# Performance work log

Measured on AMD Instinct MI355X. Metric: run time of the kernel, lower is better.

The kernel has to match this reference:

```python
import jax, jax.numpy as jnp
import numpy as np

B, TQ, TKV, NPR, H, D = 4, 1024, 1024, 5, 16, 64
IN, OUT, R, P, NT = 1024, H * D, 64, 4096, 4
KV = NPR + TKV  # prompt tokens prepended to kv sequence


def setup_inputs() -> dict:
    key = jax.random.key(0)
    ks = jax.random.split(key, 20)
    n = lambda k, shp, s: jax.random.normal(k, shp, jnp.float32) * s
    W = 0.02  # weight init scale
    return {
        "pe": n(ks[0], (P, OUT), 1.0),
        "attn_output": n(ks[1], (B, TQ, OUT), 1.0),
        "q": n(ks[2], (B, H, TQ, D), 1.0),
        "kv_query": n(ks[3], (B, TKV, IN), 1.0),
        "attn_mask": jnp.zeros((TQ, KV), jnp.float32),
        "prompt": n(ks[4], (NT, NPR, IN), 1.0),
        "gates": n(ks[5], (1,), 1.0),
        "k_w1": n(ks[6], (IN, R), W), "k_w2": n(ks[7], (R, OUT), W),
        "v_w1": n(ks[8], (IN, R), W), "v_w2": n(ks[9], (R, OUT), W),
        "kp_w1": n(ks[10], (OUT, R), W), "kp_w2": n(ks[11], (R, OUT), W),
        "qp_w1": n(ks[12], (OUT, R), W), "qp_w2": n(ks[13], (R, OUT), W),
        "indices_a": jax.random.randint(ks[14], (B, TQ), 0, P),
        "indices_b": jax.random.randint(ks[15], (B, TKV), 0, P),
        "task_idx": jax.random.randint(ks[16], (B,), 0, NT),
    }


def reference(pe, attn_output, q, kv_query, attn_mask, prompt, gates,
              k_w1, k_w2, v_w1, v_w2, kp_w1, kp_w2, qp_w1, qp_w2,
              indices_a, indices_b, task_idx):
    # prompt selection + concat in front of kv sequence
    pr = prompt[task_idx]                                   # [B, NPR, IN]
    kv_x = jnp.concatenate([pr, kv_query], axis=1)          # [B, KV, IN]
    # positional features; key_pos is zero-padded over the prompt slots
    key_pos = jnp.pad(pe[indices_b], ((0, 0), (NPR, 0), (0, 0)))  # [B, KV, OUT]
    # low-rank projections
    k = (kv_x @ k_w1) @ k_w2 + (key_pos @ kp_w1) @ kp_w2    # [B, KV, OUT]
    v = (kv_x @ v_w1) @ v_w2                                # [B, KV, OUT]
    q_pos = (pe[indices_a] @ qp_w1) @ qp_w2                 # [B, TQ, OUT]
    qh = q + q_pos.reshape(B, TQ, H, D).transpose(0, 2, 1, 3)
    kh = k.reshape(B, KV, H, D).transpose(0, 2, 1, 3)
    vh = v.reshape(B, KV, H, D).transpose(0, 2, 1, 3)
    scores = jnp.einsum('bhqd,bhkd->bhqk', qh, kh) / np.float32(np.sqrt(D))
    scores = scores + attn_mask[None, None]                 # 2D mask path
    w = jax.nn.softmax(scores, axis=-1)                     # dropout = identity (eval)
    out = jnp.einsum('bhqk,bhkd->bhqd', w, vh)
    out = out.transpose(0, 2, 1, 3).reshape(B, TQ, OUT)
    return out * gates + attn_output
```

## Files before the change

kernel.cpp:

```cpp
#include <hip/hip_runtime.h>
#include <hip/hip_bf16.h>

#define B_    4
#define TQ_   1024
#define TKV_  1024
#define NPR_  5
#define H_    16
#define D_    64
#define IN_   1024
#define OUT_  1024
#define R_    64
#define P_    4096
#define KV_   1029
#define KVP_  1088
#define M1_   4116
#define M1P_  4160
#define MQ_   4096
#define NKT_  17
#define NQT_  16
#define MR_   (M1P_ * R_)
#define LOG2E_ 1.4426950408889634f
#define SQ_SCALE_ (0.125f * 1.4426950408889634f)

typedef __attribute__((ext_vector_type(8))) short short8;
typedef __attribute__((ext_vector_type(4))) float f32x4;
typedef __attribute__((ext_vector_type(4))) unsigned uint4v;
typedef __attribute__((ext_vector_type(2))) unsigned uint2v;

#define MFMA(a, b, c) __builtin_amdgcn_mfma_f32_16x16x32_bf16(a, b, c, 0, 0, 0)

#define AS1 __attribute__((address_space(1)))
#define AS3 __attribute__((address_space(3)))
#define GLDS(g, l) __builtin_amdgcn_global_load_lds((const AS1 void*)(g), (AS3 void*)(l), 16, 0, 0)

static __device__ __forceinline__ short f2bf(float f) {
  unsigned u = __builtin_bit_cast(unsigned, f);
  u += 0x7fffu + ((u >> 16) & 1u);
  return (short)(u >> 16);
}
static __device__ __forceinline__ float bf2f(unsigned short u) {
  return __builtin_bit_cast(float, (unsigned)u << 16);
}
static __device__ __forceinline__ short8 zero8() {
  short8 z = {0, 0, 0, 0, 0, 0, 0, 0};
  return z;
}
static __device__ __forceinline__ unsigned cvtpk(float lo, float hi) {
  unsigned r;
  asm("v_cvt_pk_bf16_f32 %0, %1, %2" : "=v"(r) : "v"(lo), "v"(hi));
  return r;
}
static __device__ __forceinline__ float vexp2(float x) {
  float r;
  asm("v_exp_f32 %0, %1" : "=v"(r) : "v"(x));
  return r;
}
static __device__ __forceinline__ void pl32(unsigned &a, unsigned &b) {
  asm("v_permlane32_swap_b32 %0, %1" : "+v"(a), "+v"(b));
}
static __device__ __forceinline__ void pl16(unsigned &a, unsigned &b) {
  asm("v_permlane16_swap_b32 %0, %1" : "+v"(a), "+v"(b));
}
static __device__ __forceinline__ float redsum4(float x) {
  unsigned a = __builtin_bit_cast(unsigned, x), b = a;
  pl16(a, b);
  x = __builtin_bit_cast(float, a) + __builtin_bit_cast(float, b);
  a = b = __builtin_bit_cast(unsigned, x);
  pl32(a, b);
  return __builtin_bit_cast(float, a) + __builtin_bit_cast(float, b);
}
static __device__ __forceinline__ void cd2bfrag(const f32x4 (&s)[4], short8 &p0, short8 &p1) {
  unsigned u00 = cvtpk(s[0][0], s[0][1]), u01 = cvtpk(s[0][2], s[0][3]);
  unsigned u10 = cvtpk(s[1][0], s[1][1]), u11 = cvtpk(s[1][2], s[1][3]);
  unsigned u20 = cvtpk(s[2][0], s[2][1]), u21 = cvtpk(s[2][2], s[2][3]);
  unsigned u30 = cvtpk(s[3][0], s[3][1]), u31 = cvtpk(s[3][2], s[3][3]);
  pl32(u00, u10); pl32(u01, u11); pl32(u20, u30); pl32(u21, u31);
  pl16(u00, u10); pl16(u01, u11); pl16(u20, u30); pl16(u21, u31);
  uint4v w0 = {u00, u01, u10, u11};
  uint4v w1 = {u20, u21, u30, u31};
  p0 = __builtin_bit_cast(short8, w0);
  p1 = __builtin_bit_cast(short8, w1);
}
static __device__ __forceinline__ short8 sum4pack(const unsigned short* p) {
  f32x4 lo = {0, 0, 0, 0}, hi = {0, 0, 0, 0};
#pragma unroll
  for (int c = 0; c < 4; ++c) {
    short8 v = *(const short8*)(p + (size_t)c * MR_);
#pragma unroll
    for (int j = 0; j < 4; ++j) {
      lo[j] += bf2f((unsigned short)v[j]);
      hi[j] += bf2f((unsigned short)v[j + 4]);
    }
  }
  uint4v u = {cvtpk(lo[0], lo[1]), cvtpk(lo[2], lo[3]),
              cvtpk(hi[0], hi[1]), cvtpk(hi[2], hi[3])};
  return __builtin_bit_cast(short8, u);
}

__global__ __launch_bounds__(256) void prep(
    const float* __restrict__ kw1, const float* __restrict__ vw1,
    const float* __restrict__ kpw1, const float* __restrict__ qpw1,
    const float* __restrict__ kw2, const float* __restrict__ vw2,
    const float* __restrict__ kpw2, const float* __restrict__ qpw2,
    const float* __restrict__ mask, const float* __restrict__ pe,
    short* __restrict__ w1t, short* __restrict__ w2t,
    short* __restrict__ pebf, int* __restrict__ mflags) {
  int bid = blockIdx.x;
  if (bid < 64) {
    int tid = bid * 256 + threadIdx.x;
    const float* w1s[4] = {kw1, vw1, kpw1, qpw1};
    const float* w2s[4] = {kw2, vw2, kpw2, qpw2};
    for (int i = tid; i < 4 * R_ * IN_; i += 64 * 256) {
      int m = i >> 16, p = i & 65535, r = p >> 10, k = p & 1023;
      w1t[i] = f2bf(w1s[m][k * R_ + r]);
    }
    for (int i = tid; i < 4 * OUT_ * R_; i += 64 * 256) {
      int m = i >> 16, p = i & 65535, o = p >> 6, r = p & 63;
      w2t[i] = f2bf(w2s[m][r * OUT_ + o]);
    }
  } else if (bid < 336) {
    int t = bid - 64;
    int qt = t / NKT_, kt = t % NKT_;
    int nz = 0;
    for (int it = 0; it < 16; ++it) {
      int e = it * 256 + threadIdx.x;
      int rr = e >> 6, cc = e & 63;
      int kv = kt * 64 + cc;
      if (kv < KV_) {
        float v = mask[(size_t)(qt * 64 + rr) * KV_ + kv];
        nz |= (v != 0.0f);
      }
    }
    __shared__ int snz[4];
    unsigned long long bv = __ballot(nz);
    if ((threadIdx.x & 63) == 0) snz[threadIdx.x >> 6] = (bv != 0ULL);
    __syncthreads();
    if (threadIdx.x == 0) mflags[t] = snz[0] | snz[1] | snz[2] | snz[3];
  } else {
    int pb = bid - 336;
#pragma unroll
    for (int it = 0; it < 8; ++it) {
      int i = pb * 16384 + it * 2048 + threadIdx.x * 8;
      f32x4 a0 = *(const f32x4*)(pe + i);
      f32x4 a1 = *(const f32x4*)(pe + i + 4);
      uint4v u = {cvtpk(a0[0], a0[1]), cvtpk(a0[2], a0[3]),
                  cvtpk(a1[0], a1[1]), cvtpk(a1[2], a1[3])};
      *(uint4v*)(pebf + i) = u;
    }
  }
}

__global__ __launch_bounds__(256) void stage1(
    const float* __restrict__ prompt, const float* __restrict__ kv_query,
    const short* __restrict__ pebf, const int* __restrict__ indices_a,
    const int* __restrict__ indices_b, const int* __restrict__ task_idx,
    const short* __restrict__ w1t, unsigned short* __restrict__ part) {
  int which = blockIdx.z;
  int chunk = blockIdx.y;
  int mbase = blockIdx.x * 64;
  int lane = threadIdx.x & 63, wave = threadIdx.x >> 6;
  int lrow = lane & 15, lg = lane >> 4;
  int row = mbase + wave * 16 + lrow;

  const float* asrc_f = nullptr;
  const short* asrc_b = nullptr;
  if (which == 0) {
    int r = min(row, M1_ - 1);
    int b = r / KV_, t = r - b * KV_;
    asrc_f = (t < NPR_) ? prompt + (size_t)(task_idx[b] * NPR_ + t) * IN_
                        : kv_query + (size_t)(b * TKV_ + t - NPR_) * IN_;
  } else if (which == 1) {
    int r = min(row, M1_ - 1);
    int b = r / KV_, t = r - b * KV_;
    if (t >= NPR_) asrc_b = pebf + (size_t)indices_b[b * TKV_ + t - NPR_] * OUT_;
  } else {
    int r = min(row, MQ_ - 1);
    asrc_b = pebf + (size_t)indices_a[r] * OUT_;
  }
  const short* bt0 = w1t + (size_t)((which == 0) ? 0 : (which == 1) ? 2 : 3) * (R_ * IN_);
  const short* bt1 = w1t + (size_t)1 * (R_ * IN_);
  int k0base = chunk * 256;

  const f32x4 fz = {0, 0, 0, 0};
  f32x4 acc0[4], acc1[4];
#pragma unroll
  for (int f = 0; f < 4; ++f) { acc0[f] = fz; acc1[f] = fz; }

#pragma unroll
  for (int ks = 0; ks < 8; ++ks) {
    int kc = k0base + ks * 32 + lg * 8;
    short8 bdat;
    if (which == 0) {
      f32x4 a0 = *(const f32x4*)(asrc_f + kc);
      f32x4 a1 = *(const f32x4*)(asrc_f + kc + 4);
      uint4v au = {cvtpk(a0[0], a0[1]), cvtpk(a0[2], a0[3]),
                   cvtpk(a1[0], a1[1]), cvtpk(a1[2], a1[3])};
      bdat = __builtin_bit_cast(short8, au);
    } else {
      bdat = asrc_b ? *(const short8*)(asrc_b + kc) : zero8();
    }
#pragma unroll
    for (int f = 0; f < 4; ++f) {
      short8 w0 = *(const short8*)(bt0 + (size_t)(f * 16 + lrow) * IN_ + kc);
      acc0[f] = MFMA(w0, bdat, acc0[f]);
      if (which == 0) {
        short8 w1f = *(const short8*)(bt1 + (size_t)(f * 16 + lrow) * IN_ + kc);
        acc1[f] = MFMA(w1f, bdat, acc1[f]);
      }
    }
  }
  int o0 = (which == 0) ? 0 : (which == 1) ? 2 : 3;
  size_t mrow = (size_t)(mbase + wave * 16 + lrow) * R_;
  unsigned short* p0 = part + (size_t)(o0 * 4 + chunk) * MR_ + mrow;
#pragma unroll
  for (int f = 0; f < 4; ++f) {
    uint2v w = {cvtpk(acc0[f][0], acc0[f][1]), cvtpk(acc0[f][2], acc0[f][3])};
    *(uint2v*)(p0 + f * 16 + lg * 4) = w;
  }
  if (which == 0) {
    unsigned short* p1 = part + (size_t)(4 + chunk) * MR_ + mrow;
#pragma unroll
    for (int f = 0; f < 4; ++f) {
      uint2v w = {cvtpk(acc1[f][0], acc1[f][1]), cvtpk(acc1[f][2], acc1[f][3])};
      *(uint2v*)(p1 + f * 16 + lg * 4) = w;
    }
  }
}

__global__ __launch_bounds__(256) void stage2(
    const unsigned short* __restrict__ part, const short* __restrict__ w2t,
    short* __restrict__ kbf, short* __restrict__ vtb, short* __restrict__ tqs) {
  int L = blockIdx.x;
  int lane = threadIdx.x & 63, wave = threadIdx.x >> 6;
  int lrow = lane & 15, lg = lane >> 4;
  const f32x4 fz = {0, 0, 0, 0};

  if (L < 272) {
    int virt = (L & 7) * 34 + (L >> 3);
    int mt = virt >> 2, nh = virt & 3;
    int orow = mt * 64 + wave * 16 + lrow;
    int ob = orow / KVP_, okv = orow - ob * KVP_;
    bool valid = (okv < KV_);
    int kt = okv >> 6, rin = okv & 63;
    int prow = ob * KV_ + min(okv, KV_ - 1);
    short8 b1[2], b2[2];
#pragma unroll
    for (int ks = 0; ks < 2; ++ks) {
      int kc = ks * 32 + lg * 8;
      b1[ks] = valid ? sum4pack(part + (size_t)prow * R_ + kc) : zero8();
      b2[ks] = valid ? sum4pack(part + (size_t)8 * MR_ + (size_t)prow * R_ + kc) : zero8();
    }
    const short* w2k  = w2t;
    const short* w2kp = w2t + (size_t)2 * (OUT_ * R_);
    int sw = (rin & 7) << 3;
#pragma unroll
    for (int i = 0; i < 4; ++i) {
      int nbase = (nh * 4 + i) * 64;
      int h = nbase >> 6;
      f32x4 acc[4];
#pragma unroll
      for (int f = 0; f < 4; ++f) acc[f] = fz;
#pragma unroll
      for (int ks = 0; ks < 2; ++ks) {
        int kc = ks * 32 + lg * 8;
#pragma unroll
        for (int f = 0; f < 4; ++f) {
          short8 aK  = *(const short8*)(w2k  + (size_t)(nbase + f * 16 + lrow) * R_ + kc);
          short8 aKP = *(const short8*)(w2kp + (size_t)(nbase + f * 16 + lrow) * R_ + kc);
          acc[f] = MFMA(aK,  b1[ks], acc[f]);
          acc[f] = MFMA(aKP, b2[ks], acc[f]);
        }
      }
      size_t tb = ((size_t)((ob * H_ + h) * NKT_ + kt) << 12);
#pragma unroll
      for (int f = 0; f < 4; ++f) {
        float v0 = valid ? acc[f][0] : 0.f, v1 = valid ? acc[f][1] : 0.f;
        float v2 = valid ? acc[f][2] : 0.f, v3 = valid ? acc[f][3] : 0.f;
        uint2v w = {cvtpk(v0, v1), cvtpk(v2, v3)};
        int d0 = f * 16 + lg * 4;
        *(uint2v*)(kbf + tb + rin * 64 + (d0 ^ sw)) = w;
      }
    }
  } else if (L < 544) {
    int Lm = L - 272;
    int virt = (Lm & 7) * 34 + (Lm >> 3);
    int cb = virt >> 2, oh = virt & 3;
    short8 afr[8];
#pragma unroll
    for (int f = 0; f < 4; ++f)
#pragma unroll
      for (int ks = 0; ks < 2; ++ks) {
        int crow = cb * 64 + f * 16 + lrow;
        int bb = crow / KVP_, kvr = crow - bb * KVP_;
        afr[f * 2 + ks] = (kvr < KV_)
            ? sum4pack(part + (size_t)4 * MR_ + (size_t)(bb * KV_ + kvr) * R_ + ks * 32 + lg * 8)
            : zero8();
      }
    int bb = (cb * 64) / KVP_;
    int kvbase = cb * 64 - bb * KVP_;
    int kt = kvbase >> 6;
    const short* w2v = w2t + (size_t)1 * (OUT_ * R_);
#pragma unroll
    for (int i = 0; i < 4; ++i) {
      int obase = (oh * 4 + i) * 64;
      int o = obase + wave * 16 + lrow;
      int h = o >> 6, d = o & 63;
      f32x4 acc[4];
#pragma unroll
      for (int f = 0; f < 4; ++f) acc[f] = fz;
#pragma unroll
      for (int ks = 0; ks < 2; ++ks) {
        short8 bw = *(const short8*)(w2v + (size_t)o * R_ + ks * 32 + lg * 8);
#pragma unroll
        for (int f = 0; f < 4; ++f) acc[f] = MFMA(afr[f * 2 + ks], bw, acc[f]);
      }
      int sw = (d & 7) << 3;
      size_t tb = ((size_t)((bb * H_ + h) * NKT_ + kt) << 12);
#pragma unroll
      for (int f = 0; f < 4; ++f) {
        int kvin0 = f * 16 + lg * 4;
        float v0 = (kvbase + kvin0 + 0 < KV_) ? acc[f][0] : 0.f;
        float v1 = (kvbase + kvin0 + 1 < KV_) ? acc[f][1] : 0.f;
        float v2 = (kvbase + kvin0 + 2 < KV_) ? acc[f][2] : 0.f;
        float v3 = (kvbase + kvin0 + 3 < KV_) ? acc[f][3] : 0.f;
        uint2v w = {cvtpk(v0, v1), cvtpk(v2, v3)};
        *(uint2v*)(vtb + tb + d * 64 + (kvin0 ^ sw)) = w;
      }
    }
  } else {
    int j = L - 544;
#pragma unroll
    for (int it = 0; it < 8; ++it) {
      int idx = j * 16384 + it * 2048 + threadIdx.x * 8;
      short8 v = sum4pack(part + (size_t)12 * MR_ + idx);
      *(short8*)(tqs + idx) = v;
    }
  }
}

__global__ __launch_bounds__(256, 4) void attn(
    const short* __restrict__ tqs, const short* __restrict__ w2t,
    const float* __restrict__ qin,
    const short* __restrict__ kbf, const short* __restrict__ vtb,
    const float* __restrict__ mask, const int* __restrict__ mflags,
    const float* __restrict__ gates, const float* __restrict__ attn_in,
    float* __restrict__ out) {
  int bid = blockIdx.x;
  int xcd = bid & 7, wg = bid >> 3;
  int qt = wg & 15, g = wg >> 4;
  int grp = xcd * 8 + g;
  int h = grp & 15, b = grp >> 4;

  int lane = threadIdx.x & 63, wave = threadIdx.x >> 6;
  int lrow = lane & 15, lg = lane >> 4;
  int qbase = qt * 64 + wave * 16;

  __shared__ __align__(16) short kvls[2][2][4096];

  const short* ktile = kbf + ((size_t)grp * NKT_ << 12);
  const short* vtile = vtb + ((size_t)grp * NKT_ << 12);
  const short* kg = ktile + wave * 512 + lane * 8;
  const short* vg = vtile + wave * 512 + lane * 8;

  int sw = (lrow & 7) << 3;
  int offA = (lg * 8) ^ sw;
  int offB = (32 + lg * 8) ^ sw;
  const short* p0A = &kvls[0][0][lrow * 64 + offA];
  const short* p0B = &kvls[0][0][lrow * 64 + offB];
  const short* p1A = &kvls[1][0][lrow * 64 + offA];
  const short* p1B = &kvls[1][0][lrow * 64 + offB];
  const int* mfp = mflags + qt * NKT_;

  auto stage = [&](int t, int bsel) {
    const short* ks = kg + ((size_t)t << 12);
    const short* vs = vg + ((size_t)t << 12);
    GLDS(ks,        &kvls[bsel][0][wave * 512]);
    GLDS(ks + 2048, &kvls[bsel][0][wave * 512 + 2048]);
    GLDS(vs,        &kvls[bsel][1][wave * 512]);
    GLDS(vs + 2048, &kvls[bsel][1][wave * 512 + 2048]);
  };

  stage(0, 0);

  const f32x4 fz = {0, 0, 0, 0};
  short8 qa0, qa1;
  {
    const short* w2q = w2t + (size_t)3 * (OUT_ * R_);
    f32x4 qs[4];
#pragma unroll
    for (int f = 0; f < 4; ++f) qs[f] = fz;
#pragma unroll
    for (int ks = 0; ks < 2; ++ks) {
      short8 tqf = *(const short8*)(tqs + (size_t)(b * TQ_ + qbase + lrow) * R_ + ks * 32 + lg * 8);
#pragma unroll
      for (int f = 0; f < 4; ++f) {
        short8 wf = *(const short8*)(w2q + (size_t)(h * 64 + f * 16 + lrow) * R_ + ks * 32 + lg * 8);
        qs[f] = MFMA(wf, tqf, qs[f]);
      }
    }
    const float* qrow = qin + (size_t)(b * TQ_ + qbase + lrow) * OUT_ + h * 64;
#pragma unroll
    for (int f = 0; f < 4; ++f) {
      f32x4 qv = *(const f32x4*)(qrow + f * 16 + lg * 4);
#pragma unroll
      for (int r = 0; r < 4; ++r) qs[f][r] = (qs[f][r] + qv[r]) * SQ_SCALE_;
    }
    cd2bfrag(qs, qa0, qa1);
  }

  f32x4 oacc[4];
#pragma unroll
  for (int f = 0; f < 4; ++f) oacc[f] = fz;
  float plsum = 0.f;

  asm volatile("s_waitcnt vmcnt(0)" ::: "memory");
  __builtin_amdgcn_sched_barrier(0);
  __builtin_amdgcn_s_barrier();
  __builtin_amdgcn_sched_barrier(0);

  auto tile = [&](int t, const short* pA, const short* pB, int nbsel, bool last) {
    if (!last) {
      stage(t + 1, nbsel);
      asm volatile("s_waitcnt vmcnt(4)" ::: "memory");
    } else {
      asm volatile("s_waitcnt vmcnt(0)" ::: "memory");
    }
    __builtin_amdgcn_sched_barrier(0);
    __builtin_amdgcn_s_barrier();
    __builtin_amdgcn_sched_barrier(0);

    f32x4 s[4];
#pragma unroll
    for (int f = 0; f < 4; ++f) {
      short8 kA = *(const short8*)(pA + f * 1024);
      short8 kB = *(const short8*)(pB + f * 1024);
      s[f] = MFMA(kA, qa0, fz);
      s[f] = MFMA(kB, qa1, s[f]);
    }
    short8 vfr[8];
#pragma unroll
    for (int f = 0; f < 4; ++f) {
      vfr[f * 2 + 0] = *(const short8*)(pA + 4096 + f * 1024);
      vfr[f * 2 + 1] = *(const short8*)(pB + 4096 + f * 1024);
    }
    if (mfp[t]) {
      int kvb = t * 64;
      const float* mrp = mask + (size_t)(qbase + lrow) * KV_;
#pragma unroll
      for (int f = 0; f < 4; ++f)
#pragma unroll
        for (int r = 0; r < 4; ++r) {
          int kv = kvb + f * 16 + lg * 4 + r;
          if (kv < KV_) s[f][r] += mrp[kv] * LOG2E_;
        }
    }
    if (last) {
#pragma unroll
      for (int f = 0; f < 4; ++f)
#pragma unroll
        for (int r = 0; r < 4; ++r) {
          int kv = t * 64 + f * 16 + lg * 4 + r;
          if (kv >= KV_) s[f][r] = -1e30f;
        }
    }
#pragma unroll
    for (int f = 0; f < 4; ++f)
#pragma unroll
      for (int r = 0; r < 4; ++r) s[f][r] = vexp2(s[f][r]);
    f32x4 st = (s[0] + s[1]) + (s[2] + s[3]);
    plsum += (st[0] + st[1]) + (st[2] + st[3]);
    short8 pb0, pb1;
    cd2bfrag(s, pb0, pb1);
#pragma unroll
    for (int f = 0; f < 4; ++f) {
      oacc[f] = MFMA(vfr[f * 2 + 0], pb0, oacc[f]);
      oacc[f] = MFMA(vfr[f * 2 + 1], pb1, oacc[f]);
    }
    __builtin_amdgcn_sched_barrier(0);
    __builtin_amdgcn_s_barrier();
    __builtin_amdgcn_sched_barrier(0);
  };

#pragma unroll 1
  for (int i = 0; i < 8; ++i) {
    tile(2 * i,     p0A, p0B, 1, false);
    tile(2 * i + 1, p1A, p1B, 0, false);
  }
  tile(16, p0A, p0B, 1, true);

  float lsum = redsum4(plsum);
  float sc = gates[0] / lsum;
  const float* ain = attn_in + (size_t)(b * TQ_ + qbase + lrow) * OUT_ + h * 64;
  float* op = out + (size_t)(b * TQ_ + qbase + lrow) * OUT_ + h * 64;
#pragma unroll
  for (int f = 0; f < 4; ++f) {
    f32x4 av = *(const f32x4*)(ain + f * 16 + lg * 4);
    f32x4 ov;
#pragma unroll
    for (int r = 0; r < 4; ++r) ov[r] = oacc[f][r] * sc + av[r];
    *(f32x4*)(op + f * 16 + lg * 4) = ov;
  }
}

extern "C" void kernel_launch(void* const* d_in, const int* in_sizes, int n_in,
                              void* d_out, int out_size, void* d_ws, size_t ws_size,
                              hipStream_t stream) {
  const float* pe          = (const float*)d_in[0];
  const float* attn_output = (const float*)d_in[1];
  const float* q           = (const float*)d_in[2];
  const float* kv_query    = (const float*)d_in[3];
  const float* attn_mask   = (const float*)d_in[4];
  const float* prompt      = (const float*)d_in[5];
  const float* gates       = (const float*)d_in[6];
  const float* k_w1        = (const float*)d_in[7];
  const float* k_w2        = (const float*)d_in[8];
  const float* v_w1        = (const float*)d_in[9];
  const float* v_w2        = (const float*)d_in[10];
  const float* kp_w1       = (const float*)d_in[11];
  const float* kp_w2       = (const float*)d_in[12];
  const float* qp_w1       = (const float*)d_in[13];
  const float* qp_w2       = (const float*)d_in[14];
  const int* indices_a     = (const int*)d_in[15];
  const int* indices_b     = (const int*)d_in[16];
  const int* task_idx      = (const int*)d_in[17];
  float* out = (float*)d_out;

  const size_t TILEB = (size_t)64 * NKT_ * 4096;

  short* ws   = (short*)d_ws;
  short* w1t  = ws;
  short* w2t  = w1t + 4 * 65536;
  unsigned short* part = (unsigned short*)(w2t + 4 * 65536);
  short* tqs  = (short*)(part + (size_t)16 * MR_);
  int* mflags = (int*)(tqs + (size_t)MQ_ * R_);
  short* pebf = (short*)mflags + 1024;
  short* kbf  = pebf;
  short* vtb  = kbf + TILEB;

  hipLaunchKernelGGL(prep, dim3(592), dim3(256), 0, stream,
                     k_w1, v_w1, kp_w1, qp_w1, k_w2, v_w2, kp_w2, qp_w2,
                     attn_mask, pe, w1t, w2t, pebf, mflags);
  hipLaunchKernelGGL(stage1, dim3(65, 4, 3), dim3(256), 0, stream,
                     prompt, kv_query, pebf, indices_a, indices_b, task_idx, w1t, part);
  hipLaunchKernelGGL(stage2, dim3(560), dim3(256), 0, stream,
                     part, w2t, kbf, vtb, tqs);
  hipLaunchKernelGGL(attn, dim3(1024), dim3(256), 0, stream,
                     tqs, w2t, q, kbf, vtb, attn_mask, mflags, gates, attn_output, out);
}
```

Baseline: 105.7 us.

## Triple-buffer K/V tiles in attention with one barrier per tile

Moves the attention kernel's K/V staging from a double buffer to a triple buffer in LDS. Tile t+2 is prefetched right after a single barrier, which replaces the two barriers per tile used before. Mask flags are also preloaded into a scalar bitmask so the per-tile flag load is gone. The cost is 50% more LDS per block and launch bounds lowered from 4 to 3 waves per SIMD, which may reduce occupancy.

```diff
diff --git a/kernel.cpp b/kernel.cpp
--- a/kernel.cpp
+++ b/kernel.cpp
@@ -10,7 +10,6 @@
 #define IN_   1024
 #define OUT_  1024
 #define R_    64
-#define P_    4096
 #define KV_   1029
 #define KVP_  1088
 #define M1_   4116
@@ -338,7 +337,7 @@
   }
 }
 
-__global__ __launch_bounds__(256, 4) void attn(
+__global__ __launch_bounds__(256, 3) void attn(
     const short* __restrict__ tqs, const short* __restrict__ w2t,
     const float* __restrict__ qin,
     const short* __restrict__ kbf, const short* __restrict__ vtb,
@@ -355,7 +354,7 @@
   int lrow = lane & 15, lg = lane >> 4;
   int qbase = qt * 64 + wave * 16;
 
-  __shared__ __align__(16) short kvls[2][2][4096];
+  __shared__ __align__(16) short kvls[3][2][4096];
 
   const short* ktile = kbf + ((size_t)grp * NKT_ << 12);
   const short* vtile = vtb + ((size_t)grp * NKT_ << 12);
@@ -369,6 +368,8 @@
   const short* p0B = &kvls[0][0][lrow * 64 + offB];
   const short* p1A = &kvls[1][0][lrow * 64 + offA];
   const short* p1B = &kvls[1][0][lrow * 64 + offB];
+  const short* p2A = &kvls[2][0][lrow * 64 + offA];
+  const short* p2B = &kvls[2][0][lrow * 64 + offB];
   const int* mfp = mflags + qt * NKT_;
 
   auto stage = [&](int t, int bsel) {
@@ -381,6 +382,12 @@
   };
 
   stage(0, 0);
+  stage(1, 1);
+
+  int fl = 0;
+#pragma unroll
+  for (int t = 0; t < NKT_; ++t) fl |= (mfp[t] ? 1 : 0) << t;
+  fl = __builtin_amdgcn_readfirstlane(fl);
 
   const f32x4 fz = {0, 0, 0, 0};
   short8 qa0, qa1;
@@ -413,21 +420,13 @@
   for (int f = 0; f < 4; ++f) oacc[f] = fz;
   float plsum = 0.f;
 
-  asm volatile("s_waitcnt vmcnt(0)" ::: "memory");
-  __builtin_amdgcn_sched_barrier(0);
-  __builtin_amdgcn_s_barrier();
-  __builtin_amdgcn_sched_barrier(0);
-
-  auto tile = [&](int t, const short* pA, const short* pB, int nbsel, bool last) {
-    if (!last) {
-      stage(t + 1, nbsel);
-      asm volatile("s_waitcnt vmcnt(4)" ::: "memory");
-    } else {
-      asm volatile("s_waitcnt vmcnt(0)" ::: "memory");
-    }
+  auto tile = [&](int t, const short* pA, const short* pB, int sb, int mode) {
+    if (mode == 2) asm volatile("s_waitcnt vmcnt(0)" ::: "memory");
+    else           asm volatile("s_waitcnt vmcnt(4)" ::: "memory");
     __builtin_amdgcn_sched_barrier(0);
     __builtin_amdgcn_s_barrier();
     __builtin_amdgcn_sched_barrier(0);
+    if (mode == 0) stage(t + 2, sb);
 
     f32x4 s[4];
 #pragma unroll
@@ -443,7 +442,7 @@
       vfr[f * 2 + 0] = *(const short8*)(pA + 4096 + f * 1024);
       vfr[f * 2 + 1] = *(const short8*)(pB + 4096 + f * 1024);
     }
-    if (mfp[t]) {
+    if ((fl >> t) & 1) {
       int kvb = t * 64;
       const float* mrp = mask + (size_t)(qbase + lrow) * KV_;
 #pragma unroll
@@ -454,7 +453,7 @@
           if (kv < KV_) s[f][r] += mrp[kv] * LOG2E_;
         }
     }
-    if (last) {
+    if (mode == 2) {
 #pragma unroll
       for (int f = 0; f < 4; ++f)
 #pragma unroll
@@ -476,17 +475,16 @@
       oacc[f] = MFMA(vfr[f * 2 + 0], pb0, oacc[f]);
       oacc[f] = MFMA(vfr[f * 2 + 1], pb1, oacc[f]);
     }
-    __builtin_amdgcn_sched_barrier(0);
-    __builtin_amdgcn_s_barrier();
-    __builtin_amdgcn_sched_barrier(0);
   };
 
 #pragma unroll 1
-  for (int i = 0; i < 8; ++i) {
-    tile(2 * i,     p0A, p0B, 1, false);
-    tile(2 * i + 1, p1A, p1B, 0, false);
-  }
-  tile(16, p0A, p0B, 1, true);
+  for (int i = 0; i < 5; ++i) {
+    tile(3 * i + 0, p0A, p0B, 2, 0);
+    tile(3 * i + 1, p1A, p1B, 0, 0);
+    tile(3 * i + 2, p2A, p2B, 1, 0);
+  }
+  tile(15, p0A, p0B, 2, 1);
+  tile(16, p1A, p1B, 0, 2);
 
   float lsum = redsum4(plsum);
   float sc = gates[0] / lsum;
```

New measurement: 106.5 us. About the same (+0.8%).
